# Kernel tuning notes

Measured on AMD Instinct MI355X. Metric: run time of the kernel, lower is better.

The kernel has to match this reference:

```python
import jax, jax.numpy as jnp
import numpy as np

N_NODES = 100000


def setup_inputs() -> dict:
    key = jax.random.key(0)
    k1, k2, k3 = jax.random.split(key, 3)
    x = jax.random.normal(k1, (N_NODES, 128), dtype=jnp.float32)
    edge_index = jax.random.randint(k2, (2, 1600000), 0, N_NODES, dtype=jnp.int64)
    # GCNConv linear weight (hidden, input) and bias; PReLU slope (init 0.25 as in torch)
    W = jax.random.normal(k3, (128, 128), dtype=jnp.float32) * (1.0 / np.sqrt(128))
    b = jnp.zeros((128,), dtype=jnp.float32)
    prelu_a = jnp.full((1,), 0.25, dtype=jnp.float32)
    return {"x": x, "edge_index": edge_index, "W": W, "b": b, "prelu_a": prelu_a}


def reference(x, edge_index, W, b, prelu_a):
    n = x.shape[0]
    # add self loops (as in forward's add_self_loops)
    loop = jnp.arange(n, dtype=edge_index.dtype)
    src = jnp.concatenate([edge_index[0], loop])  # [E+N]
    dst = jnp.concatenate([edge_index[1], loop])
    # linear transform first (small GEMM), then gather/scatter on hidden dim
    h = x @ W.T  # [N, H]
    # symmetric degree normalization 1/sqrt(deg_src * deg_dst), deg = in-degree incl. self-loop
    ones = jnp.ones_like(dst, dtype=h.dtype)
    deg = jax.ops.segment_sum(ones, dst, num_segments=n)
    dinv = jnp.where(deg > 0, jax.lax.rsqrt(deg), 0.0)  # [N]
    norm = dinv[src] * dinv[dst]  # [E+N]
    msg = h[src] * norm[:, None]  # gather + scale, memory-bound
    out = jax.ops.segment_sum(msg, dst, num_segments=n) + b  # scatter-add
    # PReLU (single shared slope); dropout is identity in eval mode
    out = jnp.where(out >= 0, out, prelu_a[0] * out)
    return out
```

## Files before the change

### kernel.cpp

```cpp
#include <hip/hip_runtime.h>
#include <math.h>

#define HDIM 128
#define BSH 8
#define CAP 5120
#define CH 8192
#define GEMM_BLKS 256

typedef __attribute__((ext_vector_type(8))) short short8;
typedef __attribute__((ext_vector_type(4))) float f32x4;

__device__ inline unsigned short bf16_hi(float f) {
    return (unsigned short)(__float_as_uint(f) >> 16);
}
__device__ inline unsigned short bf16_rn(float f) {
    unsigned int u = __float_as_uint(f);
    return (unsigned short)((u + 0x7FFF + ((u >> 16) & 1)) >> 16);
}

__global__ __launch_bounds__(256) void prep_kernel(
    const float* __restrict__ W, uint4* __restrict__ Whg, uint4* __restrict__ Wlg,
    int* __restrict__ bcur) {
    const int t = threadIdx.x;
    bcur[t] = t * CAP;
    bcur[t + 256] = (t + 256) * CAP;
    for (int idx = t; idx < 2048; idx += 256) {
        const int j = idx >> 4;
        const int c = idx & 15;
        const float4* wp = (const float4*)(W + (size_t)j * HDIM + c * 8);
        float4 va = wp[0], vb = wp[1];
        float vs[8] = {va.x, va.y, va.z, va.w, vb.x, vb.y, vb.z, vb.w};
        unsigned short h[8], l[8];
        #pragma unroll
        for (int k = 0; k < 8; ++k) {
            h[k] = bf16_hi(vs[k]);
            float hf = __uint_as_float((unsigned int)h[k] << 16);
            l[k] = bf16_hi(vs[k] - hf);
        }
        uint4 hch, lch;
        hch.x = (unsigned int)h[0] | ((unsigned int)h[1] << 16);
        hch.y = (unsigned int)h[2] | ((unsigned int)h[3] << 16);
        hch.z = (unsigned int)h[4] | ((unsigned int)h[5] << 16);
        hch.w = (unsigned int)h[6] | ((unsigned int)h[7] << 16);
        lch.x = (unsigned int)l[0] | ((unsigned int)l[1] << 16);
        lch.y = (unsigned int)l[2] | ((unsigned int)l[3] << 16);
        lch.z = (unsigned int)l[4] | ((unsigned int)l[5] << 16);
        lch.w = (unsigned int)l[6] | ((unsigned int)l[7] << 16);
        Whg[idx] = hch;
        Wlg[idx] = lch;
    }
}

__device__ __forceinline__ void gemm_body(
    const float* __restrict__ x, const uint4* __restrict__ Whg,
    const uint4* __restrict__ Wlg, unsigned short* __restrict__ gb, int n,
    int g0, int g1, int bid, int nblk) {
    const int t = threadIdx.x;
    const int wave = t >> 6;
    const int lane = t & 63;
    const int q = lane >> 4;
    const int m = lane & 15;

    for (int grp = g0 + bid; grp < g1; grp += nblk) {
        const int rowbase = (grp << 7) + (wave << 5);

        f32x4 acc[2][8];
        #pragma unroll
        for (int mt = 0; mt < 2; ++mt)
            #pragma unroll
            for (int ct = 0; ct < 8; ++ct)
                acc[mt][ct] = (f32x4){0.f, 0.f, 0.f, 0.f};

        #pragma unroll
        for (int kk = 0; kk < 4; ++kk) {
            short8 ah[2], al[2];
            #pragma unroll
            for (int mt = 0; mt < 2; ++mt) {
                const int r = rowbase + (mt << 4) + m;
                float vs[8];
                if (r < n) {
                    const float4* xp = (const float4*)(x + (size_t)r * HDIM + (kk << 5) + (q << 3));
                    float4 va = xp[0], vb = xp[1];
                    vs[0] = va.x; vs[1] = va.y; vs[2] = va.z; vs[3] = va.w;
                    vs[4] = vb.x; vs[5] = vb.y; vs[6] = vb.z; vs[7] = vb.w;
                } else {
                    #pragma unroll
                    for (int k = 0; k < 8; ++k) vs[k] = 0.f;
                }
                #pragma unroll
                for (int k = 0; k < 8; ++k) {
                    unsigned short h = bf16_hi(vs[k]);
                    float hf = __uint_as_float((unsigned int)h << 16);
                    unsigned short lo = bf16_hi(vs[k] - hf);
                    ah[mt][k] = (short)h;
                    al[mt][k] = (short)lo;
                }
            }
            #pragma unroll
            for (int ct = 0; ct < 8; ++ct) {
                const int nn = (ct << 4) + m;
                const int fidx = (nn << 4) | ((kk << 2) + q);
                short8 bh = *(const short8*)&Whg[fidx];
                short8 bl = *(const short8*)&Wlg[fidx];
                #pragma unroll
                for (int mt = 0; mt < 2; ++mt) {
                    acc[mt][ct] = __builtin_amdgcn_mfma_f32_16x16x32_bf16(ah[mt], bh, acc[mt][ct], 0, 0, 0);
                    acc[mt][ct] = __builtin_amdgcn_mfma_f32_16x16x32_bf16(al[mt], bh, acc[mt][ct], 0, 0, 0);
                    acc[mt][ct] = __builtin_amdgcn_mfma_f32_16x16x32_bf16(ah[mt], bl, acc[mt][ct], 0, 0, 0);
                }
            }
        }

        #pragma unroll
        for (int mt = 0; mt < 2; ++mt) {
            #pragma unroll
            for (int rr = 0; rr < 4; ++rr) {
                const int grow = rowbase + (mt << 4) + (q << 2) + rr;
                if (grow < n) {
                    unsigned short* gp = gb + (size_t)grow * HDIM + m;
                    #pragma unroll
                    for (int ct = 0; ct < 8; ++ct)
                        gp[ct << 4] = bf16_rn(acc[mt][ct][rr]);
                }
            }
        }
    }
}

__device__ __forceinline__ void binB_body(
    const int* __restrict__ ei, int E,
    int* __restrict__ bcur, unsigned int* __restrict__ eb,
    int chunk, int* hist, int* base, int* cur) {
    const int t = threadIdx.x;
    const int c0 = chunk * CH;
    hist[t] = 0;
    hist[t + 256] = 0;
    __syncthreads();

    int sv[CH / 256], dv[CH / 256];
    #pragma unroll
    for (int k = 0; k < CH / 256; ++k) {
        int e = c0 + t + (k << 8);
        if (e < E) {
            sv[k] = ei[e];
            dv[k] = ei[E + e];
            atomicAdd(&hist[dv[k] >> BSH], 1);
        } else {
            dv[k] = -1;
        }
    }
    __syncthreads();
    if (hist[t] > 0)       base[t]       = atomicAdd(&bcur[t],       hist[t]);
    if (hist[t + 256] > 0) base[t + 256] = atomicAdd(&bcur[t + 256], hist[t + 256]);
    cur[t] = 0;
    cur[t + 256] = 0;
    __syncthreads();
    #pragma unroll
    for (int k = 0; k < CH / 256; ++k) {
        if (dv[k] >= 0) {
            int bkt = dv[k] >> BSH;
            int o = atomicAdd(&cur[bkt], 1);
            eb[(size_t)base[bkt] + o] =
                ((unsigned int)(dv[k] & ((1 << BSH) - 1)) << 24) | (unsigned int)sv[k];
        }
    }
}

__global__ __launch_bounds__(256) void fuseAB_kernel(
    const int* __restrict__ ei, int E, int* __restrict__ bcur,
    unsigned int* __restrict__ eb,
    const float* __restrict__ x, const uint4* __restrict__ Whg,
    const uint4* __restrict__ Wlg, unsigned short* __restrict__ gb,
    int n, int nchunk, int ngroups) {
    __shared__ int s_a[512], s_b[512], s_c[512];
    const int bid = blockIdx.x;
    if (bid < nchunk)
        binB_body(ei, E, bcur, eb, bid, s_a, s_b, s_c);
    else
        gemm_body(x, Whg, Wlg, gb, n, 0, ngroups, bid - nchunk, GEMM_BLKS);
}

__global__ __launch_bounds__(512) void binC_kernel(
    const unsigned int* __restrict__ eb, const int* __restrict__ bcur,
    int* __restrict__ row_ptr, float* __restrict__ dinv,
    int* __restrict__ col, int n, int NB) {
    __shared__ int hist[256];
    __shared__ int cur[256];
    __shared__ int red[512];
    __shared__ int wsum[4];
    const int t = threadIdx.x;
    const int b = blockIdx.x;
    const int node0 = b << BSH;
    const size_t s0 = (size_t)b * CAP;
    const int cnt = bcur[b] - b * CAP;

    red[t] = (t < b) ? (bcur[t] - t * CAP) : 0;
    __syncthreads();
    #pragma unroll
    for (int off = 256; off > 0; off >>= 1) {
        if (t < off) red[t] += red[t + off];
        __syncthreads();
    }
    const int o0 = red[0];

    unsigned int r[CAP / 512];
    #pragma unroll
    for (int k = 0; k < CAP / 512; ++k) {
        const int e = t + (k << 9);
        r[k] = (e < cnt) ? eb[s0 + e] : 0u;
    }

    if (t < 256) hist[t] = 0;
    __syncthreads();
    #pragma unroll
    for (int k = 0; k < CAP / 512; ++k) {
        const int e = t + (k << 9);
        if (e < cnt) atomicAdd(&hist[r[k] >> 24], 1);
    }
    __syncthreads();
    const int v = (t < 256) ? hist[t] : 0;
    int x = v;
    #pragma unroll
    for (int off = 1; off < 64; off <<= 1) {
        int u = __shfl_up(x, off);
        if ((t & 63) >= off) x += u;
    }
    if (t < 256 && (t & 63) == 63) wsum[t >> 6] = x;
    __syncthreads();
    if (t < 4) {
        int y = wsum[t];
        #pragma unroll
        for (int off = 1; off < 4; off <<= 1) {
            int u = __shfl_up(y, off);
            if (t >= off) y += u;
        }
        wsum[t] = y;
    }
    __syncthreads();
    if (t < 256) {
        int excl = x - v + ((t >> 6) ? wsum[(t >> 6) - 1] : 0);
        int node = node0 + t;
        if (node < n) {
            row_ptr[node] = o0 + excl;
            dinv[node] = rsqrtf((float)v + 1.0f);
            if (node == n - 1) row_ptr[n] = o0 + excl + v;
        }
        cur[t] = o0 + excl;
    }
    __syncthreads();
    #pragma unroll
    for (int k = 0; k < CAP / 512; ++k) {
        const int e = t + (k << 9);
        if (e < cnt) {
            int pos = atomicAdd(&cur[r[k] >> 24], 1);
            col[pos] = (int)(r[k] & 0xFFFFFF);
        }
    }
}

#define EDGE_ACC(d, u) \
    a[0] = fmaf(d, __uint_as_float((u).x << 16), a[0]); \
    a[1] = fmaf(d, __uint_as_float((u).x & 0xffff0000u), a[1]); \
    a[2] = fmaf(d, __uint_as_float((u).y << 16), a[2]); \
    a[3] = fmaf(d, __uint_as_float((u).y & 0xffff0000u), a[3]); \
    a[4] = fmaf(d, __uint_as_float((u).z << 16), a[4]); \
    a[5] = fmaf(d, __uint_as_float((u).z & 0xffff0000u), a[5]); \
    a[6] = fmaf(d, __uint_as_float((u).w << 16), a[6]); \
    a[7] = fmaf(d, __uint_as_float((u).w & 0xffff0000u), a[7]);

__global__ __launch_bounds__(256) void gather_kernel(
    const int* __restrict__ row_ptr, const int* __restrict__ col,
    const uint4* __restrict__ gbr, const float* __restrict__ dinv,
    const float* __restrict__ bias, const float* __restrict__ prelu_a,
    float* __restrict__ out, int n) {
    const int wv = threadIdx.x >> 6;
    const int lane = threadIdx.x & 63;
    const int q = lane >> 4;
    const int l16 = lane & 15;
    const int i = blockIdx.x * 4 + wv;
    if (i >= n) return;

    const int beg = row_ptr[i];
    const int end = row_ptr[i + 1];
    const float di = dinv[i];

    float a[8];
    #pragma unroll
    for (int k = 0; k < 8; ++k) a[k] = 0.f;

    if (q == 0) {
        uint4 u = gbr[(size_t)i * 16 + l16];
        EDGE_ACC(di, u)
    }

    int e = beg + q;
    for (; e + 12 < end; e += 16) {
        int s0 = col[e];
        int s1 = col[e + 4];
        int s2 = col[e + 8];
        int s3 = col[e + 12];
        float d0 = dinv[s0], d1 = dinv[s1], d2 = dinv[s2], d3 = dinv[s3];
        uint4 u0 = gbr[(size_t)s0 * 16 + l16];
        uint4 u1 = gbr[(size_t)s1 * 16 + l16];
        uint4 u2 = gbr[(size_t)s2 * 16 + l16];
        uint4 u3 = gbr[(size_t)s3 * 16 + l16];
        EDGE_ACC(d0, u0)
        EDGE_ACC(d1, u1)
        EDGE_ACC(d2, u2)
        EDGE_ACC(d3, u3)
    }
    for (; e + 4 < end; e += 8) {
        int s0 = col[e];
        int s1 = col[e + 4];
        float d0 = dinv[s0], d1 = dinv[s1];
        uint4 u0 = gbr[(size_t)s0 * 16 + l16];
        uint4 u1 = gbr[(size_t)s1 * 16 + l16];
        EDGE_ACC(d0, u0)
        EDGE_ACC(d1, u1)
    }
    if (e < end) {
        int s = col[e];
        float d = dinv[s];
        uint4 u = gbr[(size_t)s * 16 + l16];
        EDGE_ACC(d, u)
    }

    #pragma unroll
    for (int k = 0; k < 8; ++k) {
        a[k] += __shfl_xor(a[k], 16);
        a[k] += __shfl_xor(a[k], 32);
    }

    const float aa = prelu_a[0];
    const int c0 = (l16 << 3) + (q << 1);
    float2 bb = *(const float2*)(bias + c0);
    float v0 = di * a[(q << 1) + 0] + bb.x;
    float v1 = di * a[(q << 1) + 1] + bb.y;
    v0 = v0 >= 0.f ? v0 : aa * v0;
    v1 = v1 >= 0.f ? v1 : aa * v1;
    *(float2*)(out + (size_t)i * HDIM + c0) = make_float2(v0, v1);
}

extern "C" void kernel_launch(void* const* d_in, const int* in_sizes, int n_in,
                              void* d_out, int out_size, void* d_ws, size_t ws_size,
                              hipStream_t stream) {
    const float* x  = (const float*)d_in[0];
    const int*   ei = (const int*)d_in[1];
    const float* W  = (const float*)d_in[2];
    const float* b  = (const float*)d_in[3];
    const float* pa = (const float*)d_in[4];

    const int n = in_sizes[0] / HDIM;
    const int E = in_sizes[1] / 2;
    const int NB = (n + (1 << BSH) - 1) >> BSH;
    const int ngroups = (n + 127) >> 7;

    float* out = (float*)d_out;

    unsigned short* gb      = (unsigned short*)d_ws;
    unsigned int*   eb      = (unsigned int*)(gb + (size_t)n * HDIM);
    uint4*          Whg     = (uint4*)(eb + (size_t)NB * CAP);
    uint4*          Wlg     = Whg + 2048;
    float*          dinv    = (float*)(Wlg + 2048);
    int*            row_ptr = (int*)(dinv + n);
    int*            col     = row_ptr + (n + 1);
    int*            bcur    = col + E;

    const int nchunk = (E + CH - 1) / CH;
    prep_kernel<<<1, 256, 0, stream>>>(W, Whg, Wlg, bcur);
    fuseAB_kernel<<<nchunk + GEMM_BLKS, 256, 0, stream>>>(ei, E, bcur, eb, x, Whg, Wlg, gb, n, nchunk, ngroups);
    binC_kernel<<<NB, 512, 0, stream>>>(eb, bcur, row_ptr, dinv, col, n, NB);
    gather_kernel<<<(n + 3) / 4, 256, 0, stream>>>(row_ptr, col, (const uint4*)gb, dinv, b, pa, out, n);
}
```

Measured before the change: 231.0 us.

## Split GEMM across binning passes to overlap with both bucket stages

The feature GEMM is split into two parts by group index. The first part runs alongside the edge-bucketing pass and the second alongside the CSR-build pass, which is merged into a new fused kernel with 256-thread blocks. The aim is to fill idle compute units during the latency-bound binC stage and shorten the serial chain. In exchange the binC body now holds twice as many registers per thread (CAP/256 entries), and the fixed split point and block counts are tuned to this input size.

```diff
diff --git a/kernel.cpp b/kernel.cpp
--- a/kernel.cpp
+++ b/kernel.cpp
@@ -5,7 +5,9 @@
 #define BSH 8
 #define CAP 5120
 #define CH 8192
-#define GEMM_BLKS 256
+#define GEMM1_BLKS 316
+#define GEMM2_BLKS 121
+#define GSPLIT 600
 
 typedef __attribute__((ext_vector_type(8))) short short8;
 typedef __attribute__((ext_vector_type(4))) float f32x4;
@@ -166,66 +168,64 @@
     }
 }
 
-__global__ __launch_bounds__(256) void fuseAB_kernel(
+__global__ __launch_bounds__(256) void fuse1_kernel(
     const int* __restrict__ ei, int E, int* __restrict__ bcur,
     unsigned int* __restrict__ eb,
     const float* __restrict__ x, const uint4* __restrict__ Whg,
     const uint4* __restrict__ Wlg, unsigned short* __restrict__ gb,
-    int n, int nchunk, int ngroups) {
+    int n, int nchunk) {
     __shared__ int s_a[512], s_b[512], s_c[512];
     const int bid = blockIdx.x;
     if (bid < nchunk)
         binB_body(ei, E, bcur, eb, bid, s_a, s_b, s_c);
     else
-        gemm_body(x, Whg, Wlg, gb, n, 0, ngroups, bid - nchunk, GEMM_BLKS);
-}
-
-__global__ __launch_bounds__(512) void binC_kernel(
+        gemm_body(x, Whg, Wlg, gb, n, 0, GSPLIT, bid - nchunk, GEMM1_BLKS);
+}
+
+__device__ __forceinline__ void binC_body(
     const unsigned int* __restrict__ eb, const int* __restrict__ bcur,
     int* __restrict__ row_ptr, float* __restrict__ dinv,
-    int* __restrict__ col, int n, int NB) {
-    __shared__ int hist[256];
-    __shared__ int cur[256];
-    __shared__ int red[512];
-    __shared__ int wsum[4];
+    int* __restrict__ col, int n, int b,
+    int* hist, int* cur, int* red, int* wsum) {
     const int t = threadIdx.x;
-    const int b = blockIdx.x;
     const int node0 = b << BSH;
     const size_t s0 = (size_t)b * CAP;
     const int cnt = bcur[b] - b * CAP;
 
-    red[t] = (t < b) ? (bcur[t] - t * CAP) : 0;
-    __syncthreads();
-    #pragma unroll
-    for (int off = 256; off > 0; off >>= 1) {
+    int part = 0;
+    for (int k = t; k < b; k += 256) part += bcur[k] - k * CAP;
+    red[t] = part;
+    __syncthreads();
+    #pragma unroll
+    for (int off = 128; off > 0; off >>= 1) {
         if (t < off) red[t] += red[t + off];
         __syncthreads();
     }
     const int o0 = red[0];
 
-    unsigned int r[CAP / 512];
-    #pragma unroll
-    for (int k = 0; k < CAP / 512; ++k) {
-        const int e = t + (k << 9);
+    unsigned int r[CAP / 256];
+    #pragma unroll
+    for (int k = 0; k < CAP / 256; ++k) {
+        const int e = t + (k << 8);
         r[k] = (e < cnt) ? eb[s0 + e] : 0u;
     }
 
-    if (t < 256) hist[t] = 0;
-    __syncthreads();
-    #pragma unroll
-    for (int k = 0; k < CAP / 512; ++k) {
-        const int e = t + (k << 9);
+    hist[t] = 0;
+    __syncthreads();
+    #pragma unroll
+    for (int k = 0; k < CAP / 256; ++k) {
+        const int e = t + (k << 8);
         if (e < cnt) atomicAdd(&hist[r[k] >> 24], 1);
     }
     __syncthreads();
-    const int v = (t < 256) ? hist[t] : 0;
+    const int v = hist[t];
     int x = v;
     #pragma unroll
     for (int off = 1; off < 64; off <<= 1) {
         int u = __shfl_up(x, off);
         if ((t & 63) >= off) x += u;
     }
-    if (t < 256 && (t & 63) == 63) wsum[t >> 6] = x;
+    if ((t & 63) == 63) wsum[t >> 6] = x;
     __syncthreads();
     if (t < 4) {
         int y = wsum[t];
@@ -237,25 +237,39 @@
         wsum[t] = y;
     }
     __syncthreads();
-    if (t < 256) {
-        int excl = x - v + ((t >> 6) ? wsum[(t >> 6) - 1] : 0);
-        int node = node0 + t;
-        if (node < n) {
-            row_ptr[node] = o0 + excl;
-            dinv[node] = rsqrtf((float)v + 1.0f);
-            if (node == n - 1) row_ptr[n] = o0 + excl + v;
-        }
-        cur[t] = o0 + excl;
-    }
-    __syncthreads();
-    #pragma unroll
-    for (int k = 0; k < CAP / 512; ++k) {
-        const int e = t + (k << 9);
+    const int excl = x - v + ((t >> 6) ? wsum[(t >> 6) - 1] : 0);
+
+    const int node = node0 + t;
+    if (node < n) {
+        row_ptr[node] = o0 + excl;
+        dinv[node] = rsqrtf((float)v + 1.0f);
+        if (node == n - 1) row_ptr[n] = o0 + excl + v;
+    }
+    cur[t] = o0 + excl;
+    __syncthreads();
+    #pragma unroll
+    for (int k = 0; k < CAP / 256; ++k) {
+        const int e = t + (k << 8);
         if (e < cnt) {
             int pos = atomicAdd(&cur[r[k] >> 24], 1);
             col[pos] = (int)(r[k] & 0xFFFFFF);
         }
     }
+}
+
+__global__ __launch_bounds__(256) void fuse2_kernel(
+    const unsigned int* __restrict__ eb, const int* __restrict__ bcur,
+    int* __restrict__ row_ptr, float* __restrict__ dinv,
+    int* __restrict__ col,
+    const float* __restrict__ x, const uint4* __restrict__ Whg,
+    const uint4* __restrict__ Wlg, unsigned short* __restrict__ gb,
+    int n, int NB, int ngroups) {
+    __shared__ int s_h[256], s_cu[256], s_rd[256], s_ws[4];
+    const int bid = blockIdx.x;
+    if (bid < NB)
+        binC_body(eb, bcur, row_ptr, dinv, col, n, bid, s_h, s_cu, s_rd, s_ws);
+    else
+        gemm_body(x, Whg, Wlg, gb, n, GSPLIT, ngroups, bid - NB, GEMM2_BLKS);
 }
 
 #define EDGE_ACC(d, u) \
@@ -368,7 +382,7 @@
 
     const int nchunk = (E + CH - 1) / CH;
     prep_kernel<<<1, 256, 0, stream>>>(W, Whg, Wlg, bcur);
-    fuseAB_kernel<<<nchunk + GEMM_BLKS, 256, 0, stream>>>(ei, E, bcur, eb, x, Whg, Wlg, gb, n, nchunk, ngroups);
-    binC_kernel<<<NB, 512, 0, stream>>>(eb, bcur, row_ptr, dinv, col, n, NB);
+    fuse1_kernel<<<nchunk + GEMM1_BLKS, 256, 0, stream>>>(ei, E, bcur, eb, x, Whg, Wlg, gb, n, nchunk);
+    fuse2_kernel<<<NB + GEMM2_BLKS, 256, 0, stream>>>(eb, bcur, row_ptr, dinv, col, x, Whg, Wlg, gb, n, NB, ngroups);
     gather_kernel<<<(n + 3) / 4, 256, 0, stream>>>(row_ptr, col, (const uint4*)gb, dinv, b, pa, out, n);
 }
```

Measured after the change: 244.0 us. 5.6% more time.
